# Optimization experiments

Measured on AMD Instinct MI355X. Metric: run time of the kernel, lower is better.

Reference implementation:

```python
import jax, jax.numpy as jnp
import numpy as np

N, E, G = 50000, 150000, 200
D, ED_IN, EH = 320, 15, 32
NB, NT = 3, 9  # conv blocks, edge types


def setup_inputs() -> dict:
    key = jax.random.key(0)
    ks = jax.random.split(key, 16)
    s = 0.02
    return {
        "x": jax.random.normal(ks[0], (N, D), jnp.float32),
        "batch": jnp.sort(jax.random.randint(ks[1], (N,), 0, G)),
        "edge_indices": jax.random.randint(ks[2], (NT, 2, E), 0, N),
        "edge_attrs": jax.random.normal(ks[3], (NT, E, ED_IN), jnp.float32),
        "W1": jax.random.normal(ks[4], (2 * D + ED_IN, EH), jnp.float32) * s,
        "b1": jnp.zeros((EH,), jnp.float32),
        "W2": jax.random.normal(ks[5], (EH, EH), jnp.float32) * s,
        "b2": jnp.zeros((EH,), jnp.float32),
        "Wq": jax.random.normal(ks[6], (NB, NT, D, D), jnp.float32) * s,
        "bq": jnp.zeros((NB, NT, D), jnp.float32),
        "Wk": jax.random.normal(ks[7], (NB, NT, D, D), jnp.float32) * s,
        "bk": jnp.zeros((NB, NT, D), jnp.float32),
        "Wv": jax.random.normal(ks[8], (NB, NT, D, D), jnp.float32) * s,
        "bv": jnp.zeros((NB, NT, D), jnp.float32),
        "We": jax.random.normal(ks[9], (NB, NT, EH, D), jnp.float32) * s,
        "be": jnp.zeros((NB, NT, D), jnp.float32),
        "Ws": jax.random.normal(ks[10], (NB, NT, D, D), jnp.float32) * s,
        "bs": jnp.zeros((NB, NT, D), jnp.float32),
        "gamma": jnp.ones((NB, D), jnp.float32),
        "beta": jnp.zeros((NB, D), jnp.float32),
    }


def _transformer_conv(x, src, dst, ea, Wq, bq, Wk, bk, Wv, bv, We, be, Ws, bs):
    # PyG TransformerConv, heads=1, edge_dim=EH, eval mode (no dropout).
    q = (x @ Wq + bq)[dst]                    # [E, D] query at destination
    e = ea @ We + be                          # [E, D] projected edge attr
    k = (x @ Wk + bk)[src] + e                # [E, D]
    v = (x @ Wv + bv)[src] + e                # [E, D]
    alpha = (q * k).sum(-1) / jnp.sqrt(jnp.float32(D))  # [E]
    amax = jax.ops.segment_max(alpha, dst, num_segments=N)
    amax = jnp.where(jnp.isfinite(amax), amax, 0.0)     # guard empty segments
    ex = jnp.exp(alpha - amax[dst])
    denom = jax.ops.segment_sum(ex, dst, num_segments=N)
    w = ex / (denom[dst] + 1e-16)
    out = jax.ops.segment_sum(w[:, None] * v, dst, num_segments=N)
    return out + x @ Ws + bs                  # root/skip connection


def _graph_layer_norm(x, batch, gamma, beta):
    # PyG gnn.norm.LayerNorm, mode='graph': normalize per graph over nodes+channels.
    cnt = jax.ops.segment_sum(jnp.ones((N,), x.dtype), batch, num_segments=G)
    norm = jnp.maximum(cnt, 1.0) * D          # elements per graph
    mean = jax.ops.segment_sum(x.sum(-1), batch, num_segments=G) / norm
    xc = x - mean[batch][:, None]
    var = jax.ops.segment_sum((xc * xc).sum(-1), batch, num_segments=G) / norm
    out = xc / jnp.sqrt(var + 1e-5)[batch][:, None]
    return out * gamma + beta


def reference(x, batch, edge_indices, edge_attrs, W1, b1, W2, b2,
              Wq, bq, Wk, bk, Wv, bv, We, be, Ws, bs, gamma, beta):
    # Edge MLP preprocessing (uses original node features x).
    new_ea = []
    for t in range(NT):
        src, dst = edge_indices[t, 0], edge_indices[t, 1]
        cat = jnp.concatenate([x[src], x[dst], edge_attrs[t]], axis=-1)  # [E, 655]
        h = jax.nn.leaky_relu(cat @ W1 + b1)
        new_ea.append(h @ W2 + b2)

    h = x
    for b in range(NB):
        acc = jnp.zeros_like(h)
        for t in range(NT):
            src, dst = edge_indices[t, 0], edge_indices[t, 1]
            acc = acc + _transformer_conv(
                h, src, dst, new_ea[t],
                Wq[b, t], bq[b, t], Wk[b, t], bk[b, t], Wv[b, t], bv[b, t],
                We[b, t], be[b, t], Ws[b, t], bs[b, t])
        x_ = jax.nn.leaky_relu(acc / 9.0)
        x_ = _graph_layer_norm(x_, batch, gamma[b], beta[b])
        h = 0.5 * (h + x_)

    return jax.ops.segment_max(h, batch, num_segments=G)  # global max pool [G, D]
```

## Files before the change

### kernel.cpp

```cpp
#include <hip/hip_runtime.h>

#define N_NODES 50000
#define N_EDGE  150000
#define N_GRAPH 200
#define DIM     320
#define EDI     15
#define EH      32
#define NBLK    3
#define NTYP    9
#define NPAD    51200
#define BPT     50
#define QLD     1000

typedef unsigned short u16;
typedef unsigned int   u32;
typedef __bf16 bf16x8 __attribute__((ext_vector_type(8)));
typedef float  f32x4  __attribute__((ext_vector_type(4)));

__device__ __forceinline__ float b2f(u16 s) {
    u32 u = ((u32)s) << 16;
    return __builtin_bit_cast(float, u);
}
__device__ __forceinline__ u16 f2b(float f) {
    u32 u = __builtin_bit_cast(u32, f);
    u = (u + 0x7fffu + ((u >> 16) & 1u)) >> 16;
    return (u16)u;
}
__device__ __forceinline__ bf16x8 ldfrag(const u16* p) {
    return __builtin_bit_cast(bf16x8, *(const uint4*)p);
}

__global__ __launch_bounds__(256) void gemm_kernel(
    const u16* __restrict__ A, int Mstride,
    const u16* __restrict__ Bst, const float* __restrict__ bias,
    u16* __restrict__ Cb, float* __restrict__ Cf,
    int ldc, int out_cols, int M, int NP, int KQ, int mode)
{
    const int tid = threadIdx.x;
    const int wave = tid >> 6, lane = tid & 63;
    const int n0 = blockIdx.x * 128, m0 = blockIdx.y * 128;
    const int wm = (wave & 1) << 6, wn = (wave >> 1) << 6;
    const int lm = lane & 15, quad = lane >> 4;

    const u16* aBase = A + ((size_t)quad * Mstride + m0 + wm + lm) * 8;
    const u16* bBase = Bst + ((size_t)quad * NP + n0 + wn + lm) * 8;
    const size_t aK = (size_t)4 * Mstride * 8;
    const size_t bK = (size_t)4 * NP * 8;

    f32x4 acc[4][4] = {};
    const int nIter = KQ >> 2;

    bf16x8 af[4], bfr[4];
#pragma unroll
    for (int mi = 0; mi < 4; ++mi) af[mi] = ldfrag(aBase + mi * 128);
#pragma unroll
    for (int ni = 0; ni < 4; ++ni) bfr[ni] = ldfrag(bBase + ni * 128);

    for (int it = 0; it < nIter - 1; ++it) {
        bf16x8 afn[4], bfn[4];
        const u16* an = aBase + (size_t)(it + 1) * aK;
        const u16* bn = bBase + (size_t)(it + 1) * bK;
#pragma unroll
        for (int mi = 0; mi < 4; ++mi) afn[mi] = ldfrag(an + mi * 128);
#pragma unroll
        for (int ni = 0; ni < 4; ++ni) bfn[ni] = ldfrag(bn + ni * 128);
#pragma unroll
        for (int mi = 0; mi < 4; ++mi)
#pragma unroll
            for (int ni = 0; ni < 4; ++ni)
                acc[mi][ni] = __builtin_amdgcn_mfma_f32_16x16x32_bf16(af[mi], bfr[ni], acc[mi][ni], 0, 0, 0);
#pragma unroll
        for (int i = 0; i < 4; ++i) { af[i] = afn[i]; bfr[i] = bfn[i]; }
    }
#pragma unroll
    for (int mi = 0; mi < 4; ++mi)
#pragma unroll
        for (int ni = 0; ni < 4; ++ni)
            acc[mi][ni] = __builtin_amdgcn_mfma_f32_16x16x32_bf16(af[mi], bfr[ni], acc[mi][ni], 0, 0, 0);

#pragma unroll
    for (int mi = 0; mi < 4; ++mi) {
        int row = m0 + wm + mi * 16 + quad * 4;
#pragma unroll
        for (int ni = 0; ni < 4; ++ni) {
            int col = n0 + wn + ni * 16 + lm;
            float bv = bias ? bias[col] : 0.f;
#pragma unroll
            for (int r = 0; r < 4; ++r) {
                int rr = row + r;
                if (rr < M && col < out_cols) {
                    float v = acc[mi][ni][r] + bv;
                    size_t off = (size_t)rr * ldc + col;
                    if (mode == 0)      Cb[off] = f2b(v);
                    else if (mode == 1) Cf[off] = v;
                    else                Cf[off] += v;
                }
            }
        }
    }
}

__global__ void k_convert_x(const float* __restrict__ x, u16* __restrict__ hb) {
    int i = blockIdx.x * 256 + threadIdx.x;
    if (i >= N_NODES * DIM) return;
    int node = i / DIM, c = i - node * DIM;
    hb[((size_t)(c >> 3) * N_NODES + node) * 8 + (c & 7)] = f2b(x[i]);
}

__global__ void k_prep_qkvW(const float* __restrict__ Wq, const float* __restrict__ Wk,
                            const float* __restrict__ Wv, u16* __restrict__ Bst) {
    int i = blockIdx.x * 256 + threadIdx.x;
    if (i >= 27 * 40 * 1024) return;
    int col = i & 1023, kq = (i >> 10) % 40, bt = i / (40 * 1024);
    if (col >= 960 && col < 993) return;
    u16 tmp[8];
    if (col >= 993) {
#pragma unroll
        for (int r = 0; r < 8; ++r) tmp[r] = 0;
    } else {
        const float* W; int c;
        if (col < 320)      { W = Wq; c = col; }
        else if (col < 640) { W = Wk; c = col - 320; }
        else                { W = Wv; c = col - 640; }
#pragma unroll
        for (int r = 0; r < 8; ++r)
            tmp[r] = f2b(W[((size_t)bt * 320 + kq * 8 + r) * 320 + c]);
    }
    *(uint4*)(&Bst[(((size_t)bt * 40 + kq) * 1024 + col) * 8]) = *(uint4*)tmp;
}

__global__ __launch_bounds__(256) void k_prep_ext(
    const float* __restrict__ Wq, const float* __restrict__ bq,
    const float* __restrict__ We, const float* __restrict__ be,
    u16* __restrict__ Bst, float* __restrict__ biasQkv)
{
    __shared__ float WeL[33 * 321];
    int bt = blockIdx.x, kt = blockIdx.y;
    for (int i = threadIdx.x; i < 33 * 320; i += 256) {
        int r = i / 320, d = i - r * 320;
        WeL[r * 321 + d] = (r < 32) ? We[((size_t)bt * 32 + r) * 320 + d]
                                    : be[(size_t)bt * 320 + d];
    }
    __syncthreads();
    if (kt < 10) {
        int k  = kt * 32 + (threadIdx.x >> 3);
        int ct = threadIdx.x & 7;
        const float* wq = Wq + ((size_t)bt * 320 + k) * 320;
        float dot[5] = {0.f, 0.f, 0.f, 0.f, 0.f};
        for (int d = 0; d < 320; ++d) {
            float w = wq[d];
            dot[0] += w * WeL[ct * 321 + d];
            dot[1] += w * WeL[(ct + 8) * 321 + d];
            dot[2] += w * WeL[(ct + 16) * 321 + d];
            dot[3] += w * WeL[(ct + 24) * 321 + d];
            dot[4] += w * WeL[32 * 321 + d];
        }
#pragma unroll
        for (int u = 0; u < 4; ++u)
            Bst[(((size_t)bt * 40 + (k >> 3)) * 1024 + 960 + ct + u * 8) * 8 + (k & 7)] = f2b(dot[u]);
        if (ct == 0)
            Bst[(((size_t)bt * 40 + (k >> 3)) * 1024 + 992) * 8 + (k & 7)] = f2b(dot[4]);
    } else {
        int c = threadIdx.x;
        if (c < 33) {
            const float* b = bq + (size_t)bt * 320;
            float s = 0.f;
            for (int d = 0; d < 320; ++d) s += b[d] * WeL[c * 321 + d];
            biasQkv[bt * 1024 + 960 + c] = s;
        }
    }
}

__global__ void k_prep_qkvB(const float* __restrict__ bq, const float* __restrict__ bk,
                            const float* __restrict__ bv, float* __restrict__ bias) {
    int i = blockIdx.x * 256 + threadIdx.x;
    if (i >= 27 * 1024) return;
    int col = i & 1023, bt = i >> 10;
    float v;
    if (col < 320)       v = bq[bt * 320 + col];
    else if (col < 640)  v = bk[bt * 320 + col - 320];
    else if (col < 960)  v = bv[bt * 320 + col - 640];
    else if (col >= 993) v = 0.f;
    else return;
    bias[i] = v;
}

__global__ void k_prep_skipW(const float* __restrict__ Ws, u16* __restrict__ Bst) {
    int i = blockIdx.x * 256 + threadIdx.x;
    if (i >= 3 * 320 * 384) return;
    int col = i % 384, k = (i / 384) % 320, b = i / (384 * 320);
    float v = 0.f;
    if (col < 320)
        for (int t = 0; t < 9; ++t)
            v += Ws[((size_t)(b * 9 + t) * 320 + k) * 320 + col];
    Bst[(((size_t)b * 40 + (k >> 3)) * 384 + col) * 8 + (k & 7)] = f2b(v);
}
__global__ void k_prep_skipB(const float* __restrict__ bs, float* __restrict__ bias) {
    int i = blockIdx.x * 256 + threadIdx.x;
    if (i >= 3 * 384) return;
    int col = i % 384, b = i / 384;
    float v = 0.f;
    if (col < 320)
        for (int t = 0; t < 9; ++t) v += bs[(b * 9 + t) * 320 + col];
    bias[i] = v;
}

__global__ void k_prep_sWe(const float* __restrict__ We, const float* __restrict__ be,
                           u16* __restrict__ Bst) {
    int i = blockIdx.x * 256 + threadIdx.x;
    if (i >= 3 * 40 * 384) return;
    int col = i % 384, kq = (i / 384) % 40, b = i / (384 * 40);
    u16 tmp[8];
#pragma unroll
    for (int r = 0; r < 8; ++r) {
        int k = kq * 8 + r;
        float v = 0.f;
        if (col < 320 && k < 306) {
            int t = k / 34, j = k - t * 34;
            int bt = b * 9 + t;
            if (j < 32)       v = We[((size_t)bt * 32 + j) * 320 + col];
            else if (j == 32) v = be[(size_t)bt * 320 + col];
        }
        tmp[r] = f2b(v);
    }
    *(uint4*)(&Bst[(((size_t)b * 40 + kq) * 384 + col) * 8]) = *(uint4*)tmp;
}

__global__ void k_prep_w1W(const float* __restrict__ W1, u16* __restrict__ Bst) {
    int i = blockIdx.x * 256 + threadIdx.x;
    if (i >= 320 * 128) return;
    int col = i & 127, k = i >> 7;
    float v = 0.f;
    if (col < 32)      v = W1[(size_t)k * 32 + col];
    else if (col < 64) v = W1[(size_t)(320 + k) * 32 + (col - 32)];
    Bst[((size_t)(k >> 3) * 128 + col) * 8 + (k & 7)] = f2b(v);
}

__global__ void k_csr_zero(int* __restrict__ cnt) {
    int i = blockIdx.x * 256 + threadIdx.x;
    if (i < NTYP * NPAD) cnt[i] = 0;
}
__global__ void k_csr_count(const int* __restrict__ eidx, int* __restrict__ cnt) {
    int i = blockIdx.x * 256 + threadIdx.x;
    if (i >= NTYP * N_EDGE) return;
    int t = i / N_EDGE, e = i - t * N_EDGE;
    int dst = eidx[(size_t)(t * 2 + 1) * N_EDGE + e];
    atomicAdd(&cnt[t * NPAD + dst], 1);
}
__global__ __launch_bounds__(1024) void k_csr_scan1(const int* __restrict__ cnt,
                                                    int* __restrict__ rowStart,
                                                    int* __restrict__ blockSum) {
    __shared__ int tmp[1024];
    int t = blockIdx.y, blk = blockIdx.x, tid = threadIdx.x;
    int idx = t * NPAD + blk * 1024 + tid;
    int v = cnt[idx];
    tmp[tid] = v;
    __syncthreads();
    for (int off = 1; off < 1024; off <<= 1) {
        int x = (tid >= off) ? tmp[tid - off] : 0;
        __syncthreads();
        tmp[tid] += x;
        __syncthreads();
    }
    rowStart[idx] = tmp[tid] - v;
    if (tid == 1023) blockSum[t * 64 + blk] = tmp[tid];
}
__global__ void k_csr_scan2(int* __restrict__ blockSum) {
    int t = threadIdx.x;
    if (t >= NTYP) return;
    int run = 0;
    for (int b = 0; b < BPT; ++b) {
        int v = blockSum[t * 64 + b];
        blockSum[t * 64 + b] = run;
        run += v;
    }
}
__global__ void k_csr_scan3(int* __restrict__ rowStart, const int* __restrict__ blockSum,
                            int* __restrict__ cursor) {
    int i = blockIdx.x * 256 + threadIdx.x;
    if (i >= NTYP * NPAD) return;
    int t = i / NPAD, n = i - t * NPAD;
    int v = rowStart[i] + blockSum[t * 64 + (n >> 10)];
    rowStart[i] = v;
    cursor[i] = v;
}
__global__ void k_csr_scatter(const int* __restrict__ eidx, int* __restrict__ cursor,
                              u16* __restrict__ sSrc, int* __restrict__ sEid) {
    int i = blockIdx.x * 256 + threadIdx.x;
    if (i >= NTYP * N_EDGE) return;
    int t = i / N_EDGE, e = i - t * N_EDGE;
    int src = eidx[(size_t)(t * 2) * N_EDGE + e];
    int dst = eidx[(size_t)(t * 2 + 1) * N_EDGE + e];
    int pos = atomicAdd(&cursor[t * NPAD + dst], 1);
    sSrc[(size_t)t * N_EDGE + pos] = (u16)src;
    sEid[(size_t)t * N_EDGE + pos] = e;
}

__global__ __launch_bounds__(256) void k_edge_mlp(
    const u16* __restrict__ Anodes, const int* __restrict__ eidx,
    const float* __restrict__ eattr, const float* __restrict__ W1,
    const float* __restrict__ b1, const float* __restrict__ W2,
    const float* __restrict__ b2, u16* __restrict__ outEa, int t)
{
    __shared__ float w1c[EDI][EH];
    __shared__ float w2s[EH][EH];
    __shared__ float b1s[EH], b2s[EH];
    int tid = threadIdx.x;
    for (int i = tid; i < EDI * EH; i += 256) w1c[i / EH][i % EH] = W1[(640 + i / EH) * EH + (i % EH)];
    for (int i = tid; i < EH * EH; i += 256) w2s[i / EH][i % EH] = W2[i];
    if (tid < EH) { b1s[tid] = b1[tid]; b2s[tid] = b2[tid]; }
    __syncthreads();

    int e = blockIdx.x * 256 + tid;
    if (e >= N_EDGE) return;
    int src = eidx[(size_t)(t * 2) * N_EDGE + e];
    int dst = eidx[(size_t)(t * 2 + 1) * N_EDGE + e];
    const float* eat = eattr + ((size_t)t * N_EDGE + e) * EDI;
    const u16* a1 = Anodes + (size_t)src * 64;
    const u16* a2 = Anodes + (size_t)dst * 64 + 32;

    float h1[EH];
#pragma unroll
    for (int j = 0; j < EH; ++j) h1[j] = b2f(a1[j]) + b2f(a2[j]) + b1s[j];
    for (int i = 0; i < EDI; ++i) {
        float v = eat[i];
#pragma unroll
        for (int j = 0; j < EH; ++j) h1[j] += v * w1c[i][j];
    }
#pragma unroll
    for (int j = 0; j < EH; ++j) h1[j] = h1[j] > 0.f ? h1[j] : 0.01f * h1[j];

    u16* orow = outEa + (size_t)e * EH;
    for (int j = 0; j < EH; ++j) {
        float o = b2s[j];
#pragma unroll
        for (int i = 0; i < EH; ++i) o += h1[i] * w2s[i][j];
        orow[j] = f2b(o);
    }
}

__global__ __launch_bounds__(256) void k_attn(
    const u16* __restrict__ qkv, const int* __restrict__ rowStart,
    const u16* __restrict__ sSrc, const int* __restrict__ sEid,
    const u16* __restrict__ ea, float* __restrict__ acc,
    u16* __restrict__ sST, int t34)
{
    int wave = threadIdx.x >> 6, lane = threadIdx.x & 63;
    int n = blockIdx.x * 4 + wave;
    if (n >= N_NODES) return;
    int eb = rowStart[n], ee = rowStart[n + 1];
    if (eb == ee) return;

    const u16* qrow = qkv + (size_t)n * QLD;
    float q[5];
#pragma unroll
    for (int c = 0; c < 5; ++c) q[c] = b2f(qrow[c * 64 + lane]);
    float qwl = (lane < 33) ? b2f(qrow[960 + lane]) : 0.f;
    float qwbe = __shfl(qwl, 32, 64);
    float qw = (lane < 32) ? qwl : 0.f;
    const float RS = 0.05590169943749474f;

    float m = -INFINITY, l = 0.f, as = 0.f;
    float av[5] = {0.f, 0.f, 0.f, 0.f, 0.f};

    int ei = eb;
    for (; ei + 2 <= ee; ei += 2) {
        int s0 = sSrc[ei], s1 = sSrc[ei + 1];
        int id0 = sEid[ei], id1 = sEid[ei + 1];
        const u16* k0 = qkv + (size_t)s0 * QLD + 320;
        const u16* k1 = qkv + (size_t)s1 * QLD + 320;
        float ea0 = (lane < 32) ? b2f(ea[(size_t)id0 * 32 + lane]) : 0.f;
        float ea1 = (lane < 32) ? b2f(ea[(size_t)id1 * 32 + lane]) : 0.f;
        float d0 = qw * ea0, d1 = qw * ea1;
#pragma unroll
        for (int c = 0; c < 5; ++c) {
            d0 += q[c] * b2f(k0[c * 64 + lane]);
            d1 += q[c] * b2f(k1[c * 64 + lane]);
        }
#pragma unroll
        for (int off = 32; off > 0; off >>= 1) {
            d0 += __shfl_xor(d0, off, 64);
            d1 += __shfl_xor(d1, off, 64);
        }
        float a0 = (d0 + qwbe) * RS, a1 = (d1 + qwbe) * RS;
        float mn = fmaxf(m, fmaxf(a0, a1));
        float sc = __expf(m - mn);
        float p0 = __expf(a0 - mn), p1 = __expf(a1 - mn);
        l = l * sc + p0 + p1;
        const u16* v0 = k0 + 320;
        const u16* v1 = k1 + 320;
#pragma unroll
        for (int c = 0; c < 5; ++c)
            av[c] = av[c] * sc + p0 * b2f(v0[c * 64 + lane]) + p1 * b2f(v1[c * 64 + lane]);
        as = as * sc + p0 * ea0 + p1 * ea1;
        m = mn;
    }
    if (ei < ee) {
        int s0 = sSrc[ei];
        int id0 = sEid[ei];
        const u16* k0 = qkv + (size_t)s0 * QLD + 320;
        float ea0 = (lane < 32) ? b2f(ea[(size_t)id0 * 32 + lane]) : 0.f;
        float d0 = qw * ea0;
#pragma unroll
        for (int c = 0; c < 5; ++c) d0 += q[c] * b2f(k0[c * 64 + lane]);
#pragma unroll
        for (int off = 32; off > 0; off >>= 1) d0 += __shfl_xor(d0, off, 64);
        float a0 = (d0 + qwbe) * RS;
        float mn = fmaxf(m, a0);
        float sc = __expf(m - mn), p0 = __expf(a0 - mn);
        l = l * sc + p0;
        const u16* v0 = k0 + 320;
#pragma unroll
        for (int c = 0; c < 5; ++c) av[c] = av[c] * sc + p0 * b2f(v0[c * 64 + lane]);
        as = as * sc + p0 * ea0;
    }

    float inv = 1.f / l;
    float* arow = acc + (size_t)n * DIM;
#pragma unroll
    for (int c = 0; c < 5; ++c) arow[c * 64 + lane] += av[c] * inv;
    if (lane < 33) {
        int k = t34 + lane;
        float sv = (lane < 32) ? as * inv : 1.f;
        sST[((size_t)(k >> 3) * N_NODES + n) * 8 + (k & 7)] = f2b(sv);
    }
}

__device__ __forceinline__ int lowerb(const int* a, int n, int v) {
    int lo = 0, hi = n;
    while (lo < hi) { int mid = (lo + hi) >> 1; if (a[mid] < v) lo = mid + 1; else hi = mid; }
    return lo;
}

__global__ __launch_bounds__(1024) void k_post(
    const float* __restrict__ acc, u16* __restrict__ hb,
    const int* __restrict__ batch, const float* __restrict__ gamma,
    const float* __restrict__ beta)
{
    int g = blockIdx.x;
    int start = lowerb(batch, N_NODES, g);
    int end   = lowerb(batch, N_NODES, g + 1);
    int cnt = end - start;
    if (cnt == 0) return;
    int i0 = start * DIM, i1 = end * DIM;

    float s = 0.f, ss = 0.f;
    for (int i = i0 + threadIdx.x; i < i1; i += 1024) {
        float v = acc[i] * (1.f / 9.f);
        v = v > 0.f ? v : 0.01f * v;
        s += v; ss += v * v;
    }
    __shared__ float rs[16], rss[16];
#pragma unroll
    for (int off = 32; off > 0; off >>= 1) { s += __shfl_xor(s, off, 64); ss += __shfl_xor(ss, off, 64); }
    int wave = threadIdx.x >> 6, lane = threadIdx.x & 63;
    if (lane == 0) { rs[wave] = s; rss[wave] = ss; }
    __syncthreads();
    if (threadIdx.x == 0) {
        float S = 0.f, SS = 0.f;
        for (int w = 0; w < 16; ++w) { S += rs[w]; SS += rss[w]; }
        float norm = (float)cnt * DIM;
        float mean = S / norm;
        float var = SS / norm - mean * mean;
        rs[0] = mean;
        rss[0] = rsqrtf(var + 1e-5f);
    }
    __syncthreads();
    float mean = rs[0], rsig = rss[0];
    for (int i = i0 + threadIdx.x; i < i1; i += 1024) {
        float v = acc[i] * (1.f / 9.f);
        v = v > 0.f ? v : 0.01f * v;
        int node = i / DIM, c = i - node * DIM;
        float o = (v - mean) * rsig * gamma[c] + beta[c];
        size_t hidx = ((size_t)(c >> 3) * N_NODES + node) * 8 + (c & 7);
        hb[hidx] = f2b(0.5f * (b2f(hb[hidx]) + o));
    }
}

__global__ __launch_bounds__(320) void k_maxpool(
    const u16* __restrict__ hb, const int* __restrict__ batch, float* __restrict__ out)
{
    int g = blockIdx.x, c = threadIdx.x;
    int start = lowerb(batch, N_NODES, g);
    int end   = lowerb(batch, N_NODES, g + 1);
    size_t base = (size_t)(c >> 3) * N_NODES * 8 + (c & 7);
    float m = -INFINITY;
    for (int n = start; n < end; ++n) m = fmaxf(m, b2f(hb[base + (size_t)n * 8]));
    out[(size_t)g * DIM + c] = m;
}

extern "C" void kernel_launch(void* const* d_in, const int* in_sizes, int n_in,
                              void* d_out, int out_size, void* d_ws, size_t ws_size,
                              hipStream_t stream)
{
    (void)in_sizes; (void)n_in; (void)out_size;
    const float* x     = (const float*)d_in[0];
    const int*   batch = (const int*)d_in[1];
    const int*   eidx  = (const int*)d_in[2];
    const float* eattr = (const float*)d_in[3];
    const float* W1 = (const float*)d_in[4];
    const float* b1 = (const float*)d_in[5];
    const float* W2 = (const float*)d_in[6];
    const float* b2 = (const float*)d_in[7];
    const float* Wq = (const float*)d_in[8];
    const float* bq = (const float*)d_in[9];
    const float* Wk = (const float*)d_in[10];
    const float* bk = (const float*)d_in[11];
    const float* Wv = (const float*)d_in[12];
    const float* bv = (const float*)d_in[13];
    const float* We = (const float*)d_in[14];
    const float* be = (const float*)d_in[15];
    const float* Ws = (const float*)d_in[16];
    const float* bs = (const float*)d_in[17];
    const float* gamma = (const float*)d_in[18];
    const float* beta  = (const float*)d_in[19];
    float* out = (float*)d_out;

    char* base = (char*)d_ws;
    size_t off = 0;
    auto carve = [&](size_t bytes) -> char* {
        char* r = base + off;
        off += (bytes + 255) & ~(size_t)255;
        return r;
    };
    u16*   hbKq    = (u16*)  carve((size_t)40 * N_NODES * 8 * 2 + 1024);
    float* acc     = (float*)carve((size_t)N_NODES * DIM * 4);
    u16*   qkv     = (u16*)  carve((size_t)N_NODES * QLD * 2);
    u16*   sST     = (u16*)  carve((size_t)40 * N_NODES * 8 * 2 + 1024);
    u16*   Anodes  = (u16*)  carve((size_t)N_NODES * 64 * 2);
    u16*   BstQkv  = (u16*)  carve((size_t)27 * 40 * 1024 * 8 * 2);
    float* biasQkv = (float*)carve((size_t)27 * 1024 * 4);
    u16*   BstSkip = (u16*)  carve((size_t)3 * 40 * 384 * 8 * 2);
    float* biasSkip= (float*)carve((size_t)3 * 384 * 4);
    u16*   BstSWe  = (u16*)  carve((size_t)3 * 40 * 384 * 8 * 2);
    u16*   BstW1   = (u16*)  carve((size_t)40 * 128 * 8 * 2);
    int*   cnt     = (int*)  carve((size_t)NTYP * NPAD * 4);
    int*   rowStart= (int*)  carve((size_t)NTYP * NPAD * 4);
    int*   blockSum= (int*)  carve((size_t)NTYP * 64 * 4);
    u16*   sSrc    = (u16*)  carve((size_t)NTYP * N_EDGE * 2);
    int*   sEid    = (int*)  carve((size_t)NTYP * N_EDGE * 4);
    size_t fixed = off;
    size_t bigBytes   = (size_t)NTYP * N_EDGE * EH * 2;
    size_t smallBytes = (size_t)N_EDGE * EH * 2;
    int bigEa = (ws_size >= fixed + bigBytes + (1u << 20)) ? 1 : 0;
    u16* newEa = (u16*)carve(bigEa ? bigBytes : smallBytes);

    k_convert_x<<<(N_NODES * DIM + 255) / 256, 256, 0, stream>>>(x, hbKq);
    k_prep_qkvW<<<(27 * 40 * 1024 + 255) / 256, 256, 0, stream>>>(Wq, Wk, Wv, BstQkv);
    k_prep_ext<<<dim3(27, 11), 256, 0, stream>>>(Wq, bq, We, be, BstQkv, biasQkv);
    k_prep_qkvB<<<(27 * 1024 + 255) / 256, 256, 0, stream>>>(bq, bk, bv, biasQkv);
    k_prep_skipW<<<(3 * 320 * 384 + 255) / 256, 256, 0, stream>>>(Ws, BstSkip);
    k_prep_skipB<<<(3 * 384 + 255) / 256, 256, 0, stream>>>(bs, biasSkip);
    k_prep_sWe<<<(3 * 40 * 384 + 255) / 256, 256, 0, stream>>>(We, be, BstSWe);
    k_prep_w1W<<<(320 * 128 + 255) / 256, 256, 0, stream>>>(W1, BstW1);

    k_csr_zero<<<(NTYP * NPAD + 255) / 256, 256, 0, stream>>>(cnt);
    k_csr_count<<<(NTYP * N_EDGE + 255) / 256, 256, 0, stream>>>(eidx, cnt);
    k_csr_scan1<<<dim3(BPT, NTYP), 1024, 0, stream>>>(cnt, rowStart, blockSum);
    k_csr_scan2<<<1, 64, 0, stream>>>(blockSum);
    k_csr_scan3<<<(NTYP * NPAD + 255) / 256, 256, 0, stream>>>(rowStart, blockSum, cnt);
    k_csr_scatter<<<(NTYP * N_EDGE + 255) / 256, 256, 0, stream>>>(eidx, cnt, sSrc, sEid);

    const int mt = (N_NODES + 127) / 128;
    const int et = (N_EDGE + 255) / 256;
    gemm_kernel<<<dim3(1, mt), 256, 0, stream>>>(hbKq, N_NODES, BstW1, nullptr,
                                                 Anodes, nullptr, 64, 64, N_NODES, 128, 40, 0);
    if (bigEa) {
        for (int t = 0; t < NTYP; ++t)
            k_edge_mlp<<<dim3(et), 256, 0, stream>>>(
                Anodes, eidx, eattr, W1, b1, W2, b2, newEa + (size_t)t * N_EDGE * EH, t);
    }

    for (int b = 0; b < NBLK; ++b) {
        gemm_kernel<<<dim3(3, mt), 256, 0, stream>>>(
            hbKq, N_NODES, BstSkip + (size_t)b * 40 * 384 * 8, biasSkip + b * 384,
            nullptr, acc, DIM, DIM, N_NODES, 384, 40, 1);
        hipMemsetAsync(sST, 0, (size_t)40 * N_NODES * 8 * 2, stream);
        for (int t = 0; t < NTYP; ++t) {
            int bt = b * NTYP + t;
            u16* eaT = bigEa ? (newEa + (size_t)t * N_EDGE * EH) : newEa;
            if (!bigEa)
                k_edge_mlp<<<dim3(et), 256, 0, stream>>>(
                    Anodes, eidx, eattr, W1, b1, W2, b2, eaT, t);
            gemm_kernel<<<dim3(8, mt), 256, 0, stream>>>(
                hbKq, N_NODES, BstQkv + (size_t)bt * 40 * 1024 * 8, biasQkv + bt * 1024,
                qkv, nullptr, QLD, 993, N_NODES, 1024, 40, 0);
            k_attn<<<dim3((N_NODES + 3) / 4), 256, 0, stream>>>(
                qkv, rowStart + t * NPAD, sSrc + (size_t)t * N_EDGE, sEid + (size_t)t * N_EDGE,
                eaT, acc, sST, t * 34);
        }
        gemm_kernel<<<dim3(3, mt), 256, 0, stream>>>(
            sST, N_NODES, BstSWe + (size_t)b * 40 * 384 * 8, nullptr,
            nullptr, acc, DIM, DIM, N_NODES, 384, 40, 2);
        k_post<<<N_GRAPH, 1024, 0, stream>>>(acc, hbKq, batch,
                                             gamma + b * DIM, beta + b * DIM);
    }
    k_maxpool<<<N_GRAPH, 320, 0, stream>>>(hbKq, batch, out);
}
```

Measured before the change: 6.259 ms.

## Stage GEMM tiles through LDS with direct loads and vectorize attention gathers

The GEMM kernel now double-buffers A/B tiles in shared memory using global_load_lds_dwordx4 direct-to-LDS loads, and waits plus barriers once per K step. Before, each wave loaded its fragments straight from global memory into registers. The attention kernel now reads q, k, v and the acc row with 8-byte and 16-byte vector loads for the first 256 columns, plus a scalar load for the remaining 64. This cuts the number of memory instructions per gathered row. The trade-off is extra LDS use and a barrier in every GEMM iteration, and the direct-to-LDS path relies on inline asm setting m0.

```diff
diff --git a/kernel.cpp b/kernel.cpp
--- a/kernel.cpp
+++ b/kernel.cpp
@@ -21,13 +21,20 @@
     u32 u = ((u32)s) << 16;
     return __builtin_bit_cast(float, u);
 }
+__device__ __forceinline__ float b2f_lo(u32 u) { return __builtin_bit_cast(float, u << 16); }
+__device__ __forceinline__ float b2f_hi(u32 u) { return __builtin_bit_cast(float, u & 0xffff0000u); }
 __device__ __forceinline__ u16 f2b(float f) {
     u32 u = __builtin_bit_cast(u32, f);
     u = (u + 0x7fffu + ((u >> 16) & 1u)) >> 16;
     return (u16)u;
 }
-__device__ __forceinline__ bf16x8 ldfrag(const u16* p) {
-    return __builtin_bit_cast(bf16x8, *(const uint4*)p);
+
+__device__ __forceinline__ void gll16(const u16* g, u32 ldsAddr) {
+    u32 m0v = (u32)__builtin_amdgcn_readfirstlane((int)ldsAddr);
+    asm volatile("s_mov_b32 m0, %0\n\t"
+                 "global_load_lds_dwordx4 %1, off"
+                 :: "s"(m0v), "v"((unsigned long long)(size_t)g)
+                 : "memory");
 }
 
 __global__ __launch_bounds__(256) void gemm_kernel(
@@ -42,41 +49,51 @@
     const int wm = (wave & 1) << 6, wn = (wave >> 1) << 6;
     const int lm = lane & 15, quad = lane >> 4;
 
-    const u16* aBase = A + ((size_t)quad * Mstride + m0 + wm + lm) * 8;
-    const u16* bBase = Bst + ((size_t)quad * NP + n0 + wn + lm) * 8;
-    const size_t aK = (size_t)4 * Mstride * 8;
-    const size_t bK = (size_t)4 * NP * 8;
+    __shared__ uint4 smem[2][2][512];
+    const u32 ldsBase = (u32)(size_t)&smem[0][0][0];
 
     f32x4 acc[4][4] = {};
     const int nIter = KQ >> 2;
 
-    bf16x8 af[4], bfr[4];
-#pragma unroll
-    for (int mi = 0; mi < 4; ++mi) af[mi] = ldfrag(aBase + mi * 128);
-#pragma unroll
-    for (int ni = 0; ni < 4; ++ni) bfr[ni] = ldfrag(bBase + ni * 128);
-
-    for (int it = 0; it < nIter - 1; ++it) {
-        bf16x8 afn[4], bfn[4];
-        const u16* an = aBase + (size_t)(it + 1) * aK;
-        const u16* bn = bBase + (size_t)(it + 1) * bK;
-#pragma unroll
-        for (int mi = 0; mi < 4; ++mi) afn[mi] = ldfrag(an + mi * 128);
-#pragma unroll
-        for (int ni = 0; ni < 4; ++ni) bfn[ni] = ldfrag(bn + ni * 128);
+    auto stage = [&](int s, int buf) {
+        const int c0 = s << 2;
+        const u32 bufBase = ldsBase + (u32)buf * 16384u;
+#pragma unroll
+        for (int u = 0; u < 2; ++u) {
+            const int i = wave + (u << 2);
+            const int chunk = i >> 1, half = (i & 1) << 6;
+            const u16* ga = A + ((size_t)(c0 + chunk) * Mstride + m0 + half + lane) * 8;
+            gll16(ga, bufBase + (u32)i * 1024u);
+            const u16* gb = Bst + ((size_t)(c0 + chunk) * NP + n0 + half + lane) * 8;
+            gll16(gb, bufBase + 8192u + (u32)i * 1024u);
+        }
+    };
+
+    stage(0, 0);
+    asm volatile("s_waitcnt vmcnt(0)" ::: "memory");
+    __syncthreads();
+
+    int cur = 0;
+    for (int s = 0; s < nIter; ++s) {
+        if (s + 1 < nIter) stage(s + 1, cur ^ 1);
+        const uint4* aT = &smem[cur][0][0];
+        const uint4* bT = &smem[cur][1][0];
+        bf16x8 af[4], bfr[4];
+#pragma unroll
+        for (int mi = 0; mi < 4; ++mi)
+            af[mi] = __builtin_bit_cast(bf16x8, aT[quad * 128 + wm + mi * 16 + lm]);
+#pragma unroll
+        for (int ni = 0; ni < 4; ++ni)
+            bfr[ni] = __builtin_bit_cast(bf16x8, bT[quad * 128 + wn + ni * 16 + lm]);
 #pragma unroll
         for (int mi = 0; mi < 4; ++mi)
 #pragma unroll
             for (int ni = 0; ni < 4; ++ni)
                 acc[mi][ni] = __builtin_amdgcn_mfma_f32_16x16x32_bf16(af[mi], bfr[ni], acc[mi][ni], 0, 0, 0);
-#pragma unroll
-        for (int i = 0; i < 4; ++i) { af[i] = afn[i]; bfr[i] = bfn[i]; }
-    }
-#pragma unroll
-    for (int mi = 0; mi < 4; ++mi)
-#pragma unroll
-        for (int ni = 0; ni < 4; ++ni)
-            acc[mi][ni] = __builtin_amdgcn_mfma_f32_16x16x32_bf16(af[mi], bfr[ni], acc[mi][ni], 0, 0, 0);
+        asm volatile("s_waitcnt vmcnt(0)" ::: "memory");
+        __syncthreads();
+        cur ^= 1;
+    }
 
 #pragma unroll
     for (int mi = 0; mi < 4; ++mi) {
@@ -352,31 +369,36 @@
     if (eb == ee) return;
 
     const u16* qrow = qkv + (size_t)n * QLD;
-    float q[5];
-#pragma unroll
-    for (int c = 0; c < 5; ++c) q[c] = b2f(qrow[c * 64 + lane]);
+    uint2 qv = *(const uint2*)(qrow + 4 * lane);
+    float q40 = b2f_lo(qv.x), q41 = b2f_hi(qv.x);
+    float q42 = b2f_lo(qv.y), q43 = b2f_hi(qv.y);
+    float q1 = b2f(qrow[256 + lane]);
     float qwl = (lane < 33) ? b2f(qrow[960 + lane]) : 0.f;
     float qwbe = __shfl(qwl, 32, 64);
     float qw = (lane < 32) ? qwl : 0.f;
     const float RS = 0.05590169943749474f;
 
     float m = -INFINITY, l = 0.f, as = 0.f;
-    float av[5] = {0.f, 0.f, 0.f, 0.f, 0.f};
+    float av0 = 0.f, av1 = 0.f, av2 = 0.f, av3 = 0.f, avt = 0.f;
 
     int ei = eb;
     for (; ei + 2 <= ee; ei += 2) {
         int s0 = sSrc[ei], s1 = sSrc[ei + 1];
         int id0 = sEid[ei], id1 = sEid[ei + 1];
-        const u16* k0 = qkv + (size_t)s0 * QLD + 320;
-        const u16* k1 = qkv + (size_t)s1 * QLD + 320;
+        const u16* kr0 = qkv + (size_t)s0 * QLD + 320;
+        const u16* kr1 = qkv + (size_t)s1 * QLD + 320;
+        uint2 k0v = *(const uint2*)(kr0 + 4 * lane);
+        uint2 k1v = *(const uint2*)(kr1 + 4 * lane);
+        float k0t = b2f(kr0[256 + lane]);
+        float k1t = b2f(kr1[256 + lane]);
         float ea0 = (lane < 32) ? b2f(ea[(size_t)id0 * 32 + lane]) : 0.f;
         float ea1 = (lane < 32) ? b2f(ea[(size_t)id1 * 32 + lane]) : 0.f;
-        float d0 = qw * ea0, d1 = qw * ea1;
-#pragma unroll
-        for (int c = 0; c < 5; ++c) {
-            d0 += q[c] * b2f(k0[c * 64 + lane]);
-            d1 += q[c] * b2f(k1[c * 64 + lane]);
-        }
+        float d0 = qw * ea0 + q1 * k0t
+                 + q40 * b2f_lo(k0v.x) + q41 * b2f_hi(k0v.x)
+                 + q42 * b2f_lo(k0v.y) + q43 * b2f_hi(k0v.y);
+        float d1 = qw * ea1 + q1 * k1t
+                 + q40 * b2f_lo(k1v.x) + q41 * b2f_hi(k1v.x)
+                 + q42 * b2f_lo(k1v.y) + q43 * b2f_hi(k1v.y);
 #pragma unroll
         for (int off = 32; off > 0; off >>= 1) {
             d0 += __shfl_xor(d0, off, 64);
@@ -387,38 +409,53 @@
         float sc = __expf(m - mn);
         float p0 = __expf(a0 - mn), p1 = __expf(a1 - mn);
         l = l * sc + p0 + p1;
-        const u16* v0 = k0 + 320;
-        const u16* v1 = k1 + 320;
-#pragma unroll
-        for (int c = 0; c < 5; ++c)
-            av[c] = av[c] * sc + p0 * b2f(v0[c * 64 + lane]) + p1 * b2f(v1[c * 64 + lane]);
+        const u16* vr0 = kr0 + 320;
+        const u16* vr1 = kr1 + 320;
+        uint2 v0v = *(const uint2*)(vr0 + 4 * lane);
+        uint2 v1v = *(const uint2*)(vr1 + 4 * lane);
+        float v0t = b2f(vr0[256 + lane]), v1t = b2f(vr1[256 + lane]);
+        av0 = av0 * sc + p0 * b2f_lo(v0v.x) + p1 * b2f_lo(v1v.x);
+        av1 = av1 * sc + p0 * b2f_hi(v0v.x) + p1 * b2f_hi(v1v.x);
+        av2 = av2 * sc + p0 * b2f_lo(v0v.y) + p1 * b2f_lo(v1v.y);
+        av3 = av3 * sc + p0 * b2f_hi(v0v.y) + p1 * b2f_hi(v1v.y);
+        avt = avt * sc + p0 * v0t + p1 * v1t;
         as = as * sc + p0 * ea0 + p1 * ea1;
         m = mn;
     }
     if (ei < ee) {
         int s0 = sSrc[ei];
         int id0 = sEid[ei];
-        const u16* k0 = qkv + (size_t)s0 * QLD + 320;
+        const u16* kr0 = qkv + (size_t)s0 * QLD + 320;
+        uint2 k0v = *(const uint2*)(kr0 + 4 * lane);
+        float k0t = b2f(kr0[256 + lane]);
         float ea0 = (lane < 32) ? b2f(ea[(size_t)id0 * 32 + lane]) : 0.f;
-        float d0 = qw * ea0;
-#pragma unroll
-        for (int c = 0; c < 5; ++c) d0 += q[c] * b2f(k0[c * 64 + lane]);
+        float d0 = qw * ea0 + q1 * k0t
+                 + q40 * b2f_lo(k0v.x) + q41 * b2f_hi(k0v.x)
+                 + q42 * b2f_lo(k0v.y) + q43 * b2f_hi(k0v.y);
 #pragma unroll
         for (int off = 32; off > 0; off >>= 1) d0 += __shfl_xor(d0, off, 64);
         float a0 = (d0 + qwbe) * RS;
         float mn = fmaxf(m, a0);
         float sc = __expf(m - mn), p0 = __expf(a0 - mn);
         l = l * sc + p0;
-        const u16* v0 = k0 + 320;
-#pragma unroll
-        for (int c = 0; c < 5; ++c) av[c] = av[c] * sc + p0 * b2f(v0[c * 64 + lane]);
+        const u16* vr0 = kr0 + 320;
+        uint2 v0v = *(const uint2*)(vr0 + 4 * lane);
+        float v0t = b2f(vr0[256 + lane]);
+        av0 = av0 * sc + p0 * b2f_lo(v0v.x);
+        av1 = av1 * sc + p0 * b2f_hi(v0v.x);
+        av2 = av2 * sc + p0 * b2f_lo(v0v.y);
+        av3 = av3 * sc + p0 * b2f_hi(v0v.y);
+        avt = avt * sc + p0 * v0t;
         as = as * sc + p0 * ea0;
     }
 
     float inv = 1.f / l;
     float* arow = acc + (size_t)n * DIM;
-#pragma unroll
-    for (int c = 0; c < 5; ++c) arow[c * 64 + lane] += av[c] * inv;
+    f32x4 pa = *(const f32x4*)(arow + 4 * lane);
+    pa[0] += av0 * inv; pa[1] += av1 * inv;
+    pa[2] += av2 * inv; pa[3] += av3 * inv;
+    *(f32x4*)(arow + 4 * lane) = pa;
+    arow[256 + lane] += avt * inv;
     if (lane < 33) {
         int k = t34 + lane;
         float sv = (lane < 32) ? as * inv : 1.f;
```

New measurement: 6.347 ms. No clear change (+1.4%).
